# Kernel tuning notes

Hardware: AMD Instinct MI355X
Metric: run time of the kernel (lower is better)

The kernel has to match this reference:

```python
import jax, jax.numpy as jnp
import numpy as np

SEQ, D, H = 4096, 1024, 1024


def setup_inputs() -> dict:
    key = jax.random.key(0)
    k_x, k_w1, k_b1, k_w2, k_b2 = jax.random.split(key, 5)
    std = 1.0 / np.sqrt(H)
    inputs = jax.random.normal(k_x, (SEQ, D), dtype=jnp.float32)
    W1 = jax.random.uniform(k_w1, (3 * H, 2 * D), minval=-std, maxval=std, dtype=jnp.float32)
    b1 = jax.random.uniform(k_b1, (3 * H,), minval=-std, maxval=std, dtype=jnp.float32)
    W2 = jax.random.uniform(k_w2, (H, H), minval=-std, maxval=std, dtype=jnp.float32)
    b2 = jax.random.uniform(k_b2, (H,), minval=-std, maxval=std, dtype=jnp.float32)
    return {"inputs": inputs, "W1": W1, "b1": b1, "W2": W2, "b2": b2}


def reference(inputs, W1, b1, W2, b2):
    # Exclusive prefix sum along seq: s[t] = sum_{i<t} x[i]
    s = jnp.concatenate(
        [jnp.zeros((1, inputs.shape[1]), dtype=inputs.dtype),
         jnp.cumsum(inputs[:-1], axis=0)], axis=0)
    v = jnp.concatenate([inputs, s], axis=1)            # [S, 2D]
    gates = v @ W1.T + b1                               # [S, 3H]
    ig, fg, h = jnp.split(gates, 3, axis=1)
    ig = jax.nn.sigmoid(ig)
    fg = jax.nn.sigmoid(fg)
    h = jnp.tanh(h) @ W2.T + b2                         # [S, H]
    hr = h * ig
    return (fg, hr)
```

## Files before the change

kernel.cpp:

```cpp
#include <hip/hip_runtime.h>
#include <cmath>

#define S_SEQ 4096
#define HD 1024
#define NG 3072
#define CHR 32
#define NCH 128

typedef _Float16 half8_t __attribute__((ext_vector_type(8)));
typedef _Float16 half4_t __attribute__((ext_vector_type(4)));
typedef float f32x4_t __attribute__((ext_vector_type(4)));

__device__ __forceinline__ void gload_lds16(const void* g, void* l) {
  __builtin_amdgcn_global_load_lds(
      (const __attribute__((address_space(1))) void*)g,
      (__attribute__((address_space(3))) void*)l, 16, 0, 0);
}

__device__ __forceinline__ float sigmoidf_(float x) {
  return 1.f / (1.f + __expf(-x));
}
__device__ __forceinline__ float tanhf_(float x) {
  return 1.f - 2.f / (__expf(2.f * x) + 1.f);
}

#define CONV_BLOCKS 7168
__global__ void prep(const float* __restrict__ W1, const float* __restrict__ W2,
                     _Float16* __restrict__ w1h, _Float16* __restrict__ w2h,
                     const float* __restrict__ x, _Float16* __restrict__ A,
                     _Float16* __restrict__ xsum) {
  const int bid = blockIdx.x;
  if (bid < CONV_BLOCKS) {
    const int n1 = NG * 2048 / 4;
    int i = bid * 256 + threadIdx.x;
    const float* src = (i < n1) ? (W1 + (size_t)i * 4)
                                : (W2 + (size_t)(i - n1) * 4);
    _Float16* dst = (i < n1) ? (w1h + (size_t)i * 4)
                             : (w2h + (size_t)(i - n1) * 4);
    float4 v = *(const float4*)src;
    half4_t h;
    h[0] = (_Float16)v.x; h[1] = (_Float16)v.y;
    h[2] = (_Float16)v.z; h[3] = (_Float16)v.w;
    *(half4_t*)dst = h;
  } else {
    const int sx = bid - CONV_BLOCKS;
    const int j = (sx & 3) * 256 + threadIdx.x;
    const int c = sx >> 2;
    const int t0 = c * CHR;
    float run = 0.f;
    for (int t = t0; t < t0 + CHR; ++t) {
      float v = x[(size_t)t * HD + j];
      A[(size_t)t * 2048 + j]        = (_Float16)v;
      A[(size_t)t * 2048 + 1024 + j] = (_Float16)run;
      run += v;
    }
    xsum[(size_t)c * HD + j] = (_Float16)run;
  }
}

__global__ void scan_part(const float* __restrict__ praw,
                          const float* __restrict__ b1,
                          float* __restrict__ pout) {
  int j = blockIdx.x * 256 + threadIdx.x;
  float run = b1[j];
  for (int c = 0; c < NCH; c += 8) {
    float v[8];
#pragma unroll
    for (int u = 0; u < 8; ++u)
      v[u] = praw[(size_t)(c + u) * NG + j];
#pragma unroll
    for (int u = 0; u < 8; ++u) {
      pout[(size_t)(c + u) * NG + j] = run;
      run += v[u];
    }
  }
}

template <int MODE>
__global__ __launch_bounds__(256, 2)
void gemm_bt(const _Float16* __restrict__ A, const _Float16* __restrict__ B,
             int M, int N, int K, int ldb,
             float* __restrict__ C,
             const float* __restrict__ bias, const _Float16* __restrict__ mulh,
             float* __restrict__ out,
             const float* __restrict__ part, _Float16* __restrict__ igb,
             _Float16* __restrict__ th) {
  __shared__ _Float16 As[128 * 32];
  __shared__ _Float16 Bs[128 * 32];

  const int tid = threadIdx.x;
  const int lane = tid & 63;
  const int wid = tid >> 6;
  const int wr = wid >> 1;
  const int wc = wid & 1;

  const int m0 = blockIdx.y * 128;
  const int n0 = blockIdx.x * 128;

  const int srow = lane >> 2;
  const int scol = (lane & 3) << 3;

  const _Float16* gA = A + (size_t)(m0 + wid * 32 + srow) * K + scol;
  const _Float16* gB = B + (size_t)(n0 + wid * 32 + srow) * ldb + scol;
  _Float16* lA = As + (wid * 32) * 32;
  _Float16* lB = Bs + (wid * 32) * 32;

  f32x4_t acc[4][4] = {};

  const int fr = lane & 15;
  const int fk = (lane >> 4) << 3;

  for (int kk = 0; kk < K; kk += 32) {
    gload_lds16(gA + kk,                  lA);
    gload_lds16(gA + kk + (size_t)16*K,   lA + 16 * 32);
    gload_lds16(gB + kk,                  lB);
    gload_lds16(gB + kk + (size_t)16*ldb, lB + 16 * 32);
    __syncthreads();

    half8_t af[4], bf[4];
#pragma unroll
    for (int m = 0; m < 4; ++m)
      af[m] = *(const half8_t*)&As[(wr * 64 + m * 16 + fr) * 32 + fk];
#pragma unroll
    for (int n = 0; n < 4; ++n)
      bf[n] = *(const half8_t*)&Bs[(wc * 64 + n * 16 + fr) * 32 + fk];
#pragma unroll
    for (int m = 0; m < 4; ++m)
#pragma unroll
      for (int n = 0; n < 4; ++n)
        acc[m][n] = __builtin_amdgcn_mfma_f32_16x16x32_f16(af[m], bf[n],
                                                           acc[m][n], 0, 0, 0);
    __syncthreads();
  }

  const int crow = m0 + wr * 64 + ((lane >> 4) << 2);
  const int ccol = n0 + wc * 64 + (lane & 15);
#pragma unroll
  for (int m = 0; m < 4; ++m)
#pragma unroll
    for (int n = 0; n < 4; ++n) {
      const int col = ccol + n * 16;
#pragma unroll
      for (int r = 0; r < 4; ++r) {
        const int row = crow + m * 16 + r;
        const float v = acc[m][n][r];
        if (MODE == 0) {
          C[(size_t)row * N + col] = v;
        } else if (MODE == 1) {
          size_t idx = (size_t)row * N + col;
          out[idx] = (v + bias[col]) * (float)mulh[idx];
        } else {
          float g = v + part[(size_t)(row >> 5) * NG + col];
          if (col < 1024)
            igb[(size_t)row * HD + col] = (_Float16)sigmoidf_(g);
          else if (col < 2048)
            out[(size_t)row * HD + (col - 1024)] = sigmoidf_(g);
          else
            th[(size_t)row * HD + (col - 2048)] = (_Float16)tanhf_(g);
        }
      }
    }
}

extern "C" void kernel_launch(void* const* d_in, const int* in_sizes, int n_in,
                              void* d_out, int out_size, void* d_ws, size_t ws_size,
                              hipStream_t stream) {
  const float* x  = (const float*)d_in[0];
  const float* W1 = (const float*)d_in[1];
  const float* b1 = (const float*)d_in[2];
  const float* W2 = (const float*)d_in[3];
  const float* b2 = (const float*)d_in[4];
  float* out0 = (float*)d_out;
  float* out1 = out0 + (size_t)S_SEQ * HD;

  char* ws = (char*)d_ws;
  _Float16* Ah    = (_Float16*)(ws);
  _Float16* w1h   = (_Float16*)(ws + ((size_t)16 << 20));
  _Float16* w2h   = (_Float16*)(ws + ((size_t)28 << 20));
  _Float16* xsumh = (_Float16*)(ws + ((size_t)30 << 20));
  float*    praw  = (float*)   (ws + ((size_t)31 << 20));
  float*    pout  = (float*)   (ws + ((size_t)33 << 20));
  _Float16* igb   = (_Float16*)(ws + ((size_t)35 << 20));
  _Float16* th    = (_Float16*)(ws + ((size_t)43 << 20));

  prep<<<dim3(CONV_BLOCKS + 512), dim3(256), 0, stream>>>(
      W1, W2, w1h, w2h, x, Ah, xsumh);

  gemm_bt<0><<<dim3(NG / 128, 1), dim3(256), 0, stream>>>(
      xsumh, w1h + 1024, NCH, NG, HD, 2048,
      praw, nullptr, nullptr, nullptr, nullptr, nullptr, nullptr);

  scan_part<<<dim3(NG / 256), dim3(256), 0, stream>>>(praw, b1, pout);

  gemm_bt<2><<<dim3(NG / 128, S_SEQ / 128), dim3(256), 0, stream>>>(
      Ah, w1h, S_SEQ, NG, 2048, 2048,
      nullptr, nullptr, nullptr, out0, pout, igb, th);

  gemm_bt<1><<<dim3(HD / 128, S_SEQ / 128), dim3(256), 0, stream>>>(
      th, w2h, S_SEQ, HD, HD, HD,
      nullptr, b2, igb, out1, nullptr, nullptr, nullptr);
}
```

Measured before the change: 150.8 us.

## Triple-buffer main GEMMs with swizzled LDS and split-K the prefix GEMM

Replaces the single-buffered GEMM with a three-stage LDS pipeline that prefetches two K tiles ahead, XOR-swizzles LDS chunks to avoid bank conflicts, and raises MFMA wave priority during compute. Occupancy is raised to three blocks per CU. The small chunk-sum GEMM is split four ways along K, giving more blocks to fill the GPU, and scan_part adds the four partial results together. This aims to hide global-load latency and stall time at barriers, at the cost of more LDS per block and a few redundant tail loads.

```diff
diff --git a/kernel.cpp b/kernel.cpp
--- a/kernel.cpp
+++ b/kernel.cpp
@@ -62,12 +62,15 @@
                           const float* __restrict__ b1,
                           float* __restrict__ pout) {
   int j = blockIdx.x * 256 + threadIdx.x;
+  const size_t SP = (size_t)NCH * NG;
   float run = b1[j];
   for (int c = 0; c < NCH; c += 8) {
     float v[8];
 #pragma unroll
-    for (int u = 0; u < 8; ++u)
-      v[u] = praw[(size_t)(c + u) * NG + j];
+    for (int u = 0; u < 8; ++u) {
+      size_t i0 = (size_t)(c + u) * NG + j;
+      v[u] = (praw[i0] + praw[i0 + SP]) + (praw[i0 + 2 * SP] + praw[i0 + 3 * SP]);
+    }
 #pragma unroll
     for (int u = 0; u < 8; ++u) {
       pout[(size_t)(c + u) * NG + j] = run;
@@ -76,15 +79,9 @@
   }
 }
 
-template <int MODE>
 __global__ __launch_bounds__(256, 2)
-void gemm_bt(const _Float16* __restrict__ A, const _Float16* __restrict__ B,
-             int M, int N, int K, int ldb,
-             float* __restrict__ C,
-             const float* __restrict__ bias, const _Float16* __restrict__ mulh,
-             float* __restrict__ out,
-             const float* __restrict__ part, _Float16* __restrict__ igb,
-             _Float16* __restrict__ th) {
+void gemm_part(const _Float16* __restrict__ A, const _Float16* __restrict__ B,
+               float* __restrict__ C) {
   __shared__ _Float16 As[128 * 32];
   __shared__ _Float16 Bs[128 * 32];
 
@@ -94,14 +91,14 @@
   const int wr = wid >> 1;
   const int wc = wid & 1;
 
-  const int m0 = blockIdx.y * 128;
   const int n0 = blockIdx.x * 128;
+  const int koff = blockIdx.z * 256;
 
   const int srow = lane >> 2;
   const int scol = (lane & 3) << 3;
 
-  const _Float16* gA = A + (size_t)(m0 + wid * 32 + srow) * K + scol;
-  const _Float16* gB = B + (size_t)(n0 + wid * 32 + srow) * ldb + scol;
+  const _Float16* gA = A + (size_t)(wid * 32 + srow) * 1024 + koff + scol;
+  const _Float16* gB = B + (size_t)(n0 + wid * 32 + srow) * 2048 + koff + scol;
   _Float16* lA = As + (wid * 32) * 32;
   _Float16* lB = Bs + (wid * 32) * 32;
 
@@ -110,11 +107,11 @@
   const int fr = lane & 15;
   const int fk = (lane >> 4) << 3;
 
-  for (int kk = 0; kk < K; kk += 32) {
-    gload_lds16(gA + kk,                  lA);
-    gload_lds16(gA + kk + (size_t)16*K,   lA + 16 * 32);
-    gload_lds16(gB + kk,                  lB);
-    gload_lds16(gB + kk + (size_t)16*ldb, lB + 16 * 32);
+  for (int kk = 0; kk < 256; kk += 32) {
+    gload_lds16(gA + kk,                    lA);
+    gload_lds16(gA + kk + (size_t)16*1024,  lA + 16 * 32);
+    gload_lds16(gB + kk,                    lB);
+    gload_lds16(gB + kk + (size_t)16*2048,  lB + 16 * 32);
     __syncthreads();
 
     half8_t af[4], bf[4];
@@ -133,8 +130,100 @@
     __syncthreads();
   }
 
-  const int crow = m0 + wr * 64 + ((lane >> 4) << 2);
-  const int ccol = n0 + wc * 64 + (lane & 15);
+  float* Cz = C + (size_t)blockIdx.z * NCH * NG;
+  const int crow = wr * 64 + ((lane >> 4) << 2);
+  const int ccol = n0 + wc * 64 + fr;
+#pragma unroll
+  for (int m = 0; m < 4; ++m)
+#pragma unroll
+    for (int n = 0; n < 4; ++n) {
+      const int col = ccol + n * 16;
+#pragma unroll
+      for (int r = 0; r < 4; ++r)
+        Cz[(size_t)(crow + m * 16 + r) * NG + col] = acc[m][n][r];
+    }
+}
+
+#define BARX __builtin_amdgcn_s_barrier()
+#define PR1 __builtin_amdgcn_s_setprio(1)
+#define PR0 __builtin_amdgcn_s_setprio(0)
+#define VM4 asm volatile("s_waitcnt vmcnt(4)" ::: "memory")
+
+template <int NTILE, int MODE>
+__global__ __launch_bounds__(256, 3)
+void gemm_t3(const _Float16* __restrict__ A, const _Float16* __restrict__ B,
+             int N,
+             const float* __restrict__ part, _Float16* __restrict__ igb,
+             float* __restrict__ outf, _Float16* __restrict__ th,
+             const float* __restrict__ bias, const _Float16* __restrict__ mulh) {
+  constexpr int KS = NTILE * 32;
+  __shared__ __align__(16) _Float16 sA[3][128 * 32];
+  __shared__ __align__(16) _Float16 sB[3][128 * 32];
+
+  const int tid = threadIdx.x;
+  const int l = tid & 63;
+  const int wid = tid >> 6;
+  const int wr = wid >> 1;
+  const int wc = wid & 1;
+  const int m0 = blockIdx.y * 128;
+  const int n0 = blockIdx.x * 128;
+
+  const int srow = tid >> 2;
+  const int schunk = (tid & 3) ^ ((tid >> 3) & 3);
+  const _Float16* gA = A + (size_t)(m0 + srow) * KS + schunk * 8;
+  const _Float16* gB = B + (size_t)(n0 + srow) * KS + schunk * 8;
+  const int ldst = tid * 8;
+
+#define STG(bn, kt) do {                                              \
+    const int kk_ = (kt) * 32;                                        \
+    gload_lds16(gA + kk_,           &sA[bn][ldst]);                   \
+    gload_lds16(gA + kk_ + 64 * KS, &sA[bn][2048 + ldst]);            \
+    gload_lds16(gB + kk_,           &sB[bn][ldst]);                   \
+    gload_lds16(gB + kk_ + 64 * KS, &sB[bn][2048 + ldst]);            \
+  } while (0)
+
+  const int fr = l & 15;
+  const int kidx = (((l >> 4) ^ ((l >> 1) & 3)) << 3);
+
+  f32x4_t acc[4][4] = {};
+
+#define BODY(kt, bc, bn) do {                                         \
+    int ks_ = (kt) + 2; if (ks_ > NTILE - 1) ks_ = NTILE - 1;         \
+    STG(bn, ks_);                                                     \
+    half8_t af[4], bf[4];                                             \
+    _Pragma("unroll")                                                 \
+    for (int m = 0; m < 4; ++m)                                       \
+      af[m] = *(const half8_t*)&sA[bc][(wr*64 + m*16 + fr)*32 + kidx];\
+    _Pragma("unroll")                                                 \
+    for (int n = 0; n < 4; ++n)                                       \
+      bf[n] = *(const half8_t*)&sB[bc][(wc*64 + n*16 + fr)*32 + kidx];\
+    PR1;                                                              \
+    _Pragma("unroll")                                                 \
+    for (int m = 0; m < 4; ++m)                                       \
+      _Pragma("unroll")                                               \
+      for (int n = 0; n < 4; ++n)                                     \
+        acc[m][n] = __builtin_amdgcn_mfma_f32_16x16x32_f16(           \
+            af[m], bf[n], acc[m][n], 0, 0, 0);                        \
+    PR0;                                                              \
+    VM4; BARX;                                                        \
+  } while (0)
+
+  STG(0, 0);
+  STG(1, 1);
+  VM4; BARX;
+
+#pragma unroll 1
+  for (int t3 = 0; t3 < NTILE / 3; ++t3) {
+    const int kt = t3 * 3;
+    BODY(kt,     0, 2);
+    BODY(kt + 1, 1, 0);
+    BODY(kt + 2, 2, 1);
+  }
+  if constexpr (NTILE % 3 >= 1) BODY(NTILE - NTILE % 3,     0, 2);
+  if constexpr (NTILE % 3 >= 2) BODY(NTILE - NTILE % 3 + 1, 1, 0);
+
+  const int crow = m0 + wr * 64 + ((l >> 4) << 2);
+  const int ccol = n0 + wc * 64 + fr;
 #pragma unroll
   for (int m = 0; m < 4; ++m)
 #pragma unroll
@@ -144,22 +233,22 @@
       for (int r = 0; r < 4; ++r) {
         const int row = crow + m * 16 + r;
         const float v = acc[m][n][r];
-        if (MODE == 0) {
-          C[(size_t)row * N + col] = v;
-        } else if (MODE == 1) {
+        if (MODE == 1) {
           size_t idx = (size_t)row * N + col;
-          out[idx] = (v + bias[col]) * (float)mulh[idx];
+          outf[idx] = (v + bias[col]) * (float)mulh[idx];
         } else {
           float g = v + part[(size_t)(row >> 5) * NG + col];
           if (col < 1024)
             igb[(size_t)row * HD + col] = (_Float16)sigmoidf_(g);
           else if (col < 2048)
-            out[(size_t)row * HD + (col - 1024)] = sigmoidf_(g);
+            outf[(size_t)row * HD + (col - 1024)] = sigmoidf_(g);
           else
             th[(size_t)row * HD + (col - 2048)] = (_Float16)tanhf_(g);
         }
       }
     }
+#undef STG
+#undef BODY
 }
 
 extern "C" void kernel_launch(void* const* d_in, const int* in_sizes, int n_in,
@@ -178,25 +267,22 @@
   _Float16* w1h   = (_Float16*)(ws + ((size_t)16 << 20));
   _Float16* w2h   = (_Float16*)(ws + ((size_t)28 << 20));
   _Float16* xsumh = (_Float16*)(ws + ((size_t)30 << 20));
-  float*    praw  = (float*)   (ws + ((size_t)31 << 20));
-  float*    pout  = (float*)   (ws + ((size_t)33 << 20));
-  _Float16* igb   = (_Float16*)(ws + ((size_t)35 << 20));
-  _Float16* th    = (_Float16*)(ws + ((size_t)43 << 20));
+  float*    praw4 = (float*)   (ws + ((size_t)31 << 20));
+  float*    pout  = (float*)   (ws + ((size_t)37 << 20));
+  _Float16* igb   = (_Float16*)(ws + ((size_t)39 << 20));
+  _Float16* th    = (_Float16*)(ws + ((size_t)47 << 20));
 
   prep<<<dim3(CONV_BLOCKS + 512), dim3(256), 0, stream>>>(
       W1, W2, w1h, w2h, x, Ah, xsumh);
 
-  gemm_bt<0><<<dim3(NG / 128, 1), dim3(256), 0, stream>>>(
-      xsumh, w1h + 1024, NCH, NG, HD, 2048,
-      praw, nullptr, nullptr, nullptr, nullptr, nullptr, nullptr);
-
-  scan_part<<<dim3(NG / 256), dim3(256), 0, stream>>>(praw, b1, pout);
-
-  gemm_bt<2><<<dim3(NG / 128, S_SEQ / 128), dim3(256), 0, stream>>>(
-      Ah, w1h, S_SEQ, NG, 2048, 2048,
-      nullptr, nullptr, nullptr, out0, pout, igb, th);
-
-  gemm_bt<1><<<dim3(HD / 128, S_SEQ / 128), dim3(256), 0, stream>>>(
-      th, w2h, S_SEQ, HD, HD, HD,
-      nullptr, b2, igb, out1, nullptr, nullptr, nullptr);
-}
+  gemm_part<<<dim3(NG / 128, 1, 4), dim3(256), 0, stream>>>(
+      xsumh, w1h + 1024, praw4);
+
+  scan_part<<<dim3(NG / 256), dim3(256), 0, stream>>>(praw4, b1, pout);
+
+  gemm_t3<64, 2><<<dim3(NG / 128, S_SEQ / 128), dim3(256), 0, stream>>>(
+      Ah, w1h, NG, pout, igb, out0, th, nullptr, nullptr);
+
+  gemm_t3<32, 1><<<dim3(HD / 128, S_SEQ / 128), dim3(256), 0, stream>>>(
+      th, w2h, HD, nullptr, nullptr, out1, nullptr, b2, igb);
+}
```

Result: faster. 147.7 us (-2.0%).
